# Optimization experiments

Hardware: AMD Instinct MI355X
Metric: run time of the kernel (lower is better)

The kernel has to match this reference:

```python
import jax, jax.numpy as jnp
import numpy as np

# Dimensions: d_model D, heads H, head dim DH (H*DH==D), resonator freqs NF, FFN rank R
B, T, D, H, DH, NF, R = 2, 1024, 1024, 16, 64, 256, 4096
EPS_LN = 1e-5
EPS_ATTN = 1e-6


def setup_inputs() -> dict:
    key = jax.random.key(0)
    ks = jax.random.split(key, 16)
    n = lambda i, shape, s=0.02: jax.random.normal(ks[i], shape, dtype=jnp.float32) * s
    return {
        "x": jax.random.normal(ks[0], (B, T, D), dtype=jnp.float32),
        # resonator input projections
        "W_amp": n(1, (D, NF)), "b_amp": jnp.zeros((NF,), jnp.float32),
        "W_phi": n(2, (D, NF)), "b_phi": jnp.zeros((NF,), jnp.float32),
        # resonator dynamics: per-frequency rotation, retention logit, firing threshold
        "omega": jax.random.uniform(ks[3], (NF,), dtype=jnp.float32, minval=0.0, maxval=float(np.pi)),
        "ret_logit": jnp.full((NF,), 2.0, jnp.float32),
        "theta": jnp.full((NF,), 0.5, jnp.float32),
        # feat_proj: 3*NF -> D
        "W_feat": n(4, (3 * NF, D)), "b_feat": jnp.zeros((D,), jnp.float32),
        # linear attention projections (BDH-GPU style, relu feature map, no out proj)
        "Wq": n(5, (D, H * DH)), "Wk": n(6, (D, H * DH)), "Wv": n(7, (D, H * DH)),
        # per-head layernorm affine
        "lnh_w": jnp.ones((H, DH), jnp.float32), "lnh_b": jnp.zeros((H, DH), jnp.float32),
        # ReLU low-rank FFN (positive_out=True)
        "W1": n(8, (D, R)), "b1": jnp.zeros((R,), jnp.float32),
        "W2": n(9, (R, D)), "b2": jnp.zeros((D,), jnp.float32),
        # final layernorm
        "ln_w": jnp.ones((D,), jnp.float32), "ln_b": jnp.zeros((D,), jnp.float32),
    }


def reference(x, W_amp, b_amp, W_phi, b_phi, omega, ret_logit, theta,
              W_feat, b_feat, Wq, Wk, Wv, lnh_w, lnh_b,
              W1, b1, W2, b2, ln_w, ln_b):
    Bb, Tt, Dd = x.shape
    # --- resonator input field: complex polar(amp, phi) ---
    amp = jax.nn.softplus(x @ W_amp + b_amp)                 # [B,T,NF]
    phi = jnp.float32(np.pi) * jnp.tanh(x @ W_phi + b_phi)   # [B,T,NF]
    u = jax.lax.complex(amp * jnp.cos(phi), amp * jnp.sin(phi))  # complex64 [B,T,NF]
    # --- sequential complex resonator recurrence (the kernel-headroom scan) ---
    decay = jax.nn.sigmoid(ret_logit)                         # [NF]
    a = jax.lax.complex(decay * jnp.cos(omega), decay * jnp.sin(omega))  # [NF] complex

    def step(X, u_t):
        pre = a * X + u_t                                     # [B,NF] complex
        g = jax.nn.sigmoid(jnp.abs(pre) - theta)              # threshold-map gate
        Xn = pre * g.astype(pre.dtype)
        return Xn, Xn

    X0 = jnp.zeros((Bb, u.shape[-1]), jnp.complex64)
    _, Xs = jax.lax.scan(step, X0, jnp.swapaxes(u, 0, 1))     # [T,B,NF]
    Xs = jnp.swapaxes(Xs, 0, 1)                               # [B,T,NF]
    feat = jnp.concatenate([Xs.real, Xs.imag, jnp.abs(Xs)], axis=-1)  # [B,T,3NF]
    h = jax.nn.relu(feat @ W_feat + b_feat)                   # pos(feat_proj(feat)) -> [B,T,D]
    # --- causal linear attention (relu feature map, cumulative KV state) ---
    q = jax.nn.relu(h @ Wq).reshape(Bb, Tt, H, DH)
    k = jax.nn.relu(h @ Wk).reshape(Bb, Tt, H, DH)
    v = (h @ Wv).reshape(Bb, Tt, H, DH)
    kv = jnp.cumsum(k[..., :, None] * v[..., None, :], axis=1)  # [B,T,H,DH,DH]
    ksum = jnp.cumsum(k, axis=1)                                 # [B,T,H,DH]
    num = jnp.einsum('bthd,bthde->bthe', q, kv)
    den = jnp.einsum('bthd,bthd->bth', q, ksum)[..., None] + EPS_ATTN
    y = num / den                                                # [B,T,H,DH]
    # --- per-head layernorm ---
    mean = y.mean(-1, keepdims=True)
    var = y.var(-1, keepdims=True)
    y = (y - mean) / jnp.sqrt(var + EPS_LN) * lnh_w + lnh_b
    y = y.reshape(Bb, Tt, H * DH)                                # [B,T,D]
    # --- ReLU low-rank FFN, positive_out ---
    y = jax.nn.relu(jax.nn.relu(y @ W1 + b1) @ W2 + b2)
    # --- residual + layernorm ---
    z = x + y
    mu = z.mean(-1, keepdims=True)
    vz = z.var(-1, keepdims=True)
    out = (z - mu) / jnp.sqrt(vz + EPS_LN) * ln_w + ln_b
    return out
```

## Files before the change

kernel.cpp:

```cpp
#include <hip/hip_runtime.h>
#include <hip/hip_bf16.h>
#include <math.h>

#ifndef M_PI_F
#define M_PI_F 3.14159265358979323846f
#endif

static constexpr int Bb = 2, Tt = 1024, Dd = 1024, Hh = 16, DHh = 64, NFf = 256, Rr = 4096;
static constexpr int Mm = Bb * Tt;
static constexpr int CHK = 64, NCHK = Tt / CHK;
static constexpr int QS = 3072;

enum Epi { EPI_NONE = 0, EPI_RELU, EPI_QKV };

typedef __attribute__((ext_vector_type(8))) short bf16x8;
typedef __attribute__((ext_vector_type(4))) float f32x4;

__device__ inline float bf2f(unsigned short u) {
  union { unsigned int i; float f; } c;
  c.i = (unsigned int)u << 16;
  return c.f;
}

__device__ inline void gload16(const short* g, short* l) {
  __builtin_amdgcn_global_load_lds(
      (const __attribute__((address_space(1))) unsigned int*)g,
      (__attribute__((address_space(3))) unsigned int*)l, 16, 0, 0);
}

#define GSTAGE(bufsel, kk0)                                           \
  _Pragma("unroll") for (int si = 0; si < 4; ++si) {                  \
    const int s = wid + si * 4;                                       \
    gload16(A + (size_t)(m0 + s * 8 + srow) * ldk + (kk0) + skk,      \
            &lA[(bufsel) * 8192 + s * 512]);                          \
    gload16(BT + (size_t)(n0 + s * 8 + srow) * ldk + (kk0) + skk,     \
            &lB[(bufsel) * 8192 + s * 512]);                          \
  }

template <int EPI, int OUTBF, int SPLITK>
__global__ __launch_bounds__(256) void gemm_mfma(const short* __restrict__ A,
                                                 const short* __restrict__ BT,
                                                 const float* __restrict__ bias,
                                                 float* __restrict__ Cf,
                                                 __hip_bfloat16* __restrict__ Cb,
                                                 int M, int N, int ldk) {
  __shared__ short lA[2 * 128 * 64];
  __shared__ short lB[2 * 128 * 64];
  const int tid = threadIdx.x;
  const int wid = tid >> 6, lane = tid & 63;

  const int nwg = gridDim.x * gridDim.y;
  const int wg = blockIdx.y * gridDim.x + blockIdx.x;
  const int qq = nwg >> 3, rr = nwg & 7;
  const int xcd = wg & 7, idx = wg >> 3;
  const int wg2 = (xcd < rr ? xcd * (qq + 1) : rr * (qq + 1) + (xcd - rr) * qq) + idx;
  const int bx = wg2 % gridDim.x, by = wg2 / gridDim.x;

  const int m0 = by * 128, n0 = bx * 128;
  const int wm = (wid >> 1) * 64, wn = (wid & 1) * 64;
  const int srow = lane >> 3;
  const int skk = (((lane & 7) ^ (lane >> 3)) << 3);

  int kstart = 0, klen = ldk;
  if (SPLITK > 1) {
    klen = ldk / SPLITK;
    kstart = blockIdx.z * klen;
    if (OUTBF)
      Cb += (size_t)blockIdx.z * M * N;
    else
      Cf += (size_t)blockIdx.z * M * N;
  }
  const int kend = kstart + klen;

  f32x4 acc[4][4] = {};

  GSTAGE(0, kstart);
  int cur = 0;
  for (int k0 = kstart; k0 < kend; k0 += 64) {
    if (k0 + 64 < kend) {
      GSTAGE(cur ^ 1, k0 + 64);
      asm volatile("s_waitcnt vmcnt(8)" ::: "memory");
    } else {
      asm volatile("s_waitcnt vmcnt(0)" ::: "memory");
    }
    asm volatile("s_barrier" ::: "memory");
    const short* bA = &lA[cur * 8192];
    const short* bB = &lB[cur * 8192];
#pragma unroll
    for (int kk = 0; kk < 2; ++kk) {
      const int krd = kk * 32 + (lane >> 4) * 8;
      const int rsel = lane & 15;
      const int kswz = krd ^ ((rsel & 7) << 3);
      bf16x8 af[4], bfr[4];
#pragma unroll
      for (int i = 0; i < 4; ++i) {
        af[i] = *(const bf16x8*)&bA[(wm + i * 16 + rsel) * 64 + kswz];
        bfr[i] = *(const bf16x8*)&bB[(wn + i * 16 + rsel) * 64 + kswz];
      }
#pragma unroll
      for (int i = 0; i < 4; ++i)
#pragma unroll
        for (int j = 0; j < 4; ++j)
          acc[i][j] = __builtin_amdgcn_mfma_f32_16x16x32_bf16(af[i], bfr[j], acc[i][j], 0, 0, 0);
    }
    asm volatile("s_barrier" ::: "memory");
    cur ^= 1;
  }

  const int crow = (lane >> 4) * 4;
  const int ccol = lane & 15;
#pragma unroll
  for (int j = 0; j < 4; ++j) {
    const int col = n0 + wn + j * 16 + ccol;
    const float bv = bias ? bias[col] : 0.f;
#pragma unroll
    for (int i = 0; i < 4; ++i) {
#pragma unroll
      for (int r = 0; r < 4; ++r) {
        float v = acc[i][j][r] + bv;
        const int row = m0 + wm + i * 16 + crow + r;
        if (EPI == EPI_QKV) {
          const float vv = (col < 2048) ? fmaxf(v, 0.f) : v;
          Cb[(size_t)row * QS + col] = __float2bfloat16(vv);
        } else {
          if (EPI == EPI_RELU) v = fmaxf(v, 0.f);
          const size_t off = (size_t)row * N + col;
          if (OUTBF)
            Cb[off] = __float2bfloat16(v);
          else
            Cf[off] = v;
        }
      }
    }
  }
}

__global__ __launch_bounds__(256) void reduce_polar(const __hip_bfloat16* __restrict__ part,
                                                    const float* __restrict__ b_amp,
                                                    const float* __restrict__ b_phi,
                                                    __hip_bfloat16* __restrict__ outr,
                                                    __hip_bfloat16* __restrict__ outi) {
  const int idx = blockIdx.x * 256 + threadIdx.x;
  const int row = idx >> 8, c = idx & 255;
  const size_t MN = (size_t)Mm * 512;
  const size_t pa = (size_t)row * 512 + c;
  const unsigned short* pu = (const unsigned short*)part;
  float a = bf2f(pu[pa]) + bf2f(pu[pa + MN]) + bf2f(pu[pa + 2 * MN]) + bf2f(pu[pa + 3 * MN]) +
            b_amp[c];
  float ph = bf2f(pu[pa + 256]) + bf2f(pu[pa + 256 + MN]) + bf2f(pu[pa + 256 + 2 * MN]) +
             bf2f(pu[pa + 256 + 3 * MN]) + b_phi[c];
  a = (a > 0.f) ? (a + log1pf(expf(-a))) : log1pf(expf(a));
  ph = M_PI_F * tanhf(ph);
  float s, co;
  sincosf(ph, &s, &co);
  outr[idx] = __float2bfloat16(a * co);
  outi[idx] = __float2bfloat16(a * s);
}

struct TCDesc {
  const float* src[8];
  __hip_bfloat16* dst[8];
  const float* x;
  __hip_bfloat16* xb;
};

__global__ __launch_bounds__(256) void transpose_cast_all(TCDesc d) {
  constexpr int KS[8] = {1024, 1024, 768, 1024, 1024, 1024, 1024, 4096};
  constexpr int NS[8] = {256, 256, 1024, 1024, 1024, 1024, 4096, 1024};
  constexpr int CUM[9] = {0, 256, 512, 1280, 2304, 3328, 4352, 8448, 12544};
  const int bid = blockIdx.x;
  if (bid >= 12544) {
    const int i = ((bid - 12544) * 256 + threadIdx.x) * 4;
    const float4 v = *(const float4*)&d.x[i];
    d.xb[i + 0] = __float2bfloat16(v.x);
    d.xb[i + 1] = __float2bfloat16(v.y);
    d.xb[i + 2] = __float2bfloat16(v.z);
    d.xb[i + 3] = __float2bfloat16(v.w);
    return;
  }
  __shared__ float tile[32][33];
  int w = 0;
#pragma unroll
  for (int i = 0; i < 8; ++i)
    if (bid >= CUM[i + 1]) w = i + 1;
  const int tlocal = bid - CUM[w];
  const int K = KS[w], N = NS[w];
  const int tilesN = N / 32;
  const int bk = (tlocal / tilesN) * 32, bn = (tlocal % tilesN) * 32;
  const float* W = d.src[w];
  __hip_bfloat16* WT = d.dst[w];
  const int tx = threadIdx.x & 31, ty = threadIdx.x >> 5;
#pragma unroll
  for (int r = 0; r < 32; r += 8) tile[ty + r][tx] = W[(size_t)(bk + ty + r) * N + bn + tx];
  __syncthreads();
#pragma unroll
  for (int r = 0; r < 32; r += 8)
    WT[(size_t)(bn + ty + r) * K + bk + tx] = __float2bfloat16(tile[tx][ty + r]);
}

static constexpr int RES_P = 16;
static constexpr int RES_TC = 128;
static constexpr int RES_W = 128;

#define RES_LOAD(buf_r, buf_i, tg)                                        \
  if ((tg) < cend) {                                                      \
    _Pragma("unroll") for (int i = 0; i < RES_P; ++i) {                   \
      buf_r[i] = __bfloat162float(ur[bbase + (size_t)((tg) + i) * NFf]);  \
      buf_i[i] = __bfloat162float(ui[bbase + (size_t)((tg) + i) * NFf]);  \
    }                                                                     \
  }

#define RES_STEP(buf_r, buf_i, tg)                                      \
  {                                                                      \
    const bool wr_ = (tg) >= cstart;                                     \
    _Pragma("unroll") for (int i = 0; i < RES_P; ++i) {                  \
      const float pr = fmaf(ar, Xr, fmaf(-ai, Xi, buf_r[i]));            \
      const float pim = fmaf(ar, Xi, fmaf(ai, Xr, buf_i[i]));            \
      const float mag = __builtin_amdgcn_sqrtf(fmaf(pr, pr, pim * pim)); \
      const float g = __builtin_amdgcn_rcpf(1.f + __expf(th - mag));     \
      Xr = pr * g;                                                       \
      Xi = pim * g;                                                      \
      if (wr_) {                                                         \
        const size_t fb = ((size_t)b * Tt + (tg) + i) * (3 * NFf);       \
        featb[fb + f] = __float2bfloat16(Xr);                            \
        featb[fb + NFf + f] = __float2bfloat16(Xi);                      \
        featb[fb + 2 * NFf + f] = __float2bfloat16(mag * g);             \
      }                                                                  \
    }                                                                    \
  }

__global__ __launch_bounds__(64) void resonator_scan(const __hip_bfloat16* __restrict__ ur,
                                                     const __hip_bfloat16* __restrict__ ui,
                                                     const float* __restrict__ omega,
                                                     const float* __restrict__ ret_logit,
                                                     const float* __restrict__ theta,
                                                     __hip_bfloat16* __restrict__ featb) {
  const int bid = blockIdx.x;
  const int tc = bid & 7;
  const int fs = (bid >> 3) & 3;
  const int b = bid >> 5;
  const int f = fs * 64 + threadIdx.x;
  const int cstart = tc * RES_TC;
  const int cend = cstart + RES_TC;
  const int tbeg = (cstart >= RES_W) ? cstart - RES_W : 0;

  const float dec = 1.f / (1.f + __expf(-ret_logit[f]));
  float so, co;
  sincosf(omega[f], &so, &co);
  const float ar = dec * co, ai = dec * so;
  const float th = theta[f];
  const size_t bbase = (size_t)b * Tt * NFf + f;
  float Xr = 0.f, Xi = 0.f;
  float Ar[RES_P], Ai[RES_P], Br[RES_P], Bi[RES_P];
  RES_LOAD(Ar, Ai, tbeg);
  for (int t0 = tbeg; t0 < cend; t0 += 2 * RES_P) {
    RES_LOAD(Br, Bi, t0 + RES_P);
    RES_STEP(Ar, Ai, t0);
    RES_LOAD(Ar, Ai, t0 + 2 * RES_P);
    RES_STEP(Br, Bi, t0 + RES_P);
  }
}

__global__ __launch_bounds__(256) void attn_chunk_kv(const __hip_bfloat16* __restrict__ k,
                                                     const __hip_bfloat16* __restrict__ v,
                                                     float* __restrict__ S,
                                                     float* __restrict__ Ksum) {
  __shared__ float Ks[64][68], Vs[64][68];
  const int g = blockIdx.x;
  const int j = g & (NCHK - 1), bh = g >> 4;
  const int b = bh >> 4, h = bh & (Hh - 1);
  const int tid = threadIdx.x;
  const size_t rowbase = (size_t)(b * Tt + j * CHK) * QS + h * DHh;
  const unsigned short* ku = (const unsigned short*)k;
  const unsigned short* vu = (const unsigned short*)v;
  for (int l = tid; l < 4096; l += 256) {
    const int s = l >> 6, d = l & 63;
    Ks[s][d] = bf2f(ku[rowbase + (size_t)s * QS + d]);
    Vs[s][d] = bf2f(vu[rowbase + (size_t)s * QS + d]);
  }
  __syncthreads();
  const int d0 = tid & 63, eb = tid >> 6, e0 = eb * 16;
  float4 acc4[4] = {};
  float ks = 0.f;
  for (int s = 0; s < 64; ++s) {
    const float kd = Ks[s][d0];
    ks += kd;
#pragma unroll
    for (int i = 0; i < 4; ++i) {
      const float4 v4 = *(const float4*)&Vs[s][e0 + 4 * i];
      acc4[i].x = fmaf(kd, v4.x, acc4[i].x);
      acc4[i].y = fmaf(kd, v4.y, acc4[i].y);
      acc4[i].z = fmaf(kd, v4.z, acc4[i].z);
      acc4[i].w = fmaf(kd, v4.w, acc4[i].w);
    }
  }
  float* Sg = S + (size_t)g * 4096 + (size_t)d0 * 64 + e0;
#pragma unroll
  for (int i = 0; i < 4; ++i) *(float4*)&Sg[4 * i] = acc4[i];
  if (eb == 0) Ksum[(size_t)g * 64 + d0] = ks;
}

__global__ __launch_bounds__(256) void attn_prefix(float* __restrict__ S,
                                                   float* __restrict__ Ksum) {
  const int bid = blockIdx.x;
  const int tid = threadIdx.x;
  if (bid < 512) {
    const int bh = bid >> 4, r = bid & 15;
    const int de = r * 256 + tid;
    const size_t base = (size_t)bh * (NCHK * 4096) + de;
    float vv[NCHK];
#pragma unroll
    for (int j = 0; j < NCHK; ++j) vv[j] = S[base + (size_t)j * 4096];
    float run = 0.f;
#pragma unroll
    for (int j = 0; j < NCHK; ++j) {
      const float tmp = vv[j];
      S[base + (size_t)j * 4096] = run;
      run += tmp;
    }
  } else {
    const int cid = (bid - 512) * 256 + tid;
    const int bh = cid >> 6, d = cid & 63;
    const size_t base = (size_t)bh * (NCHK * 64) + d;
    float vv[NCHK];
#pragma unroll
    for (int j = 0; j < NCHK; ++j) vv[j] = Ksum[base + (size_t)j * 64];
    float run = 0.f;
#pragma unroll
    for (int j = 0; j < NCHK; ++j) {
      const float tmp = vv[j];
      Ksum[base + (size_t)j * 64] = run;
      run += tmp;
    }
  }
}

__global__ __launch_bounds__(256) void attn_out(const __hip_bfloat16* __restrict__ q,
                                                const __hip_bfloat16* __restrict__ k,
                                                const __hip_bfloat16* __restrict__ v,
                                                const float* __restrict__ S,
                                                const float* __restrict__ Ksum,
                                                const float* __restrict__ lnw,
                                                const float* __restrict__ lnb,
                                                __hip_bfloat16* __restrict__ yhb) {
  __shared__ float Qt[64][65];
  __shared__ float KVP[64][68];
  __shared__ float At[64][65];
  const int g = blockIdx.x;
  const int j = g & (NCHK - 1), bh = g >> 4;
  const int b = bh >> 4, h = bh & (Hh - 1);
  const int tid = threadIdx.x;
  const size_t rowbase = (size_t)(b * Tt + j * CHK) * QS + h * DHh;
  const unsigned short* qu = (const unsigned short*)q;
  const unsigned short* ku = (const unsigned short*)k;
  const unsigned short* vu = (const unsigned short*)v;
  for (int l = tid; l < 4096; l += 256) {
    const int s = l >> 6, d = l & 63;
    Qt[d][s] = bf2f(qu[rowbase + (size_t)s * QS + d]);
    KVP[s][d] = bf2f(ku[rowbase + (size_t)s * QS + d]);
  }
  __syncthreads();
  const int t = tid >> 2, sg = tid & 3;
  const float* pk = Ksum + (size_t)g * 64;
  float adot[16] = {};
  float qpk = 0.f;
  for (int c = 0; c < 16; ++c) {
    const float q0 = Qt[4 * c + 0][t], q1 = Qt[4 * c + 1][t];
    const float q2 = Qt[4 * c + 2][t], q3 = Qt[4 * c + 3][t];
    const float4 pk4 = *(const float4*)&pk[4 * c];
    qpk = fmaf(q0, pk4.x, fmaf(q1, pk4.y, fmaf(q2, pk4.z, fmaf(q3, pk4.w, qpk))));
#pragma unroll
    for (int i = 0; i < 16; ++i) {
      const float4 k4 = *(const float4*)&KVP[sg * 16 + i][4 * c];
      adot[i] = fmaf(q0, k4.x, fmaf(q1, k4.y, fmaf(q2, k4.z, fmaf(q3, k4.w, adot[i]))));
    }
  }
  float rs = 0.f;
#pragma unroll
  for (int i = 0; i < 16; ++i) {
    if (sg * 16 + i > t) adot[i] = 0.f;
    rs += adot[i];
  }
  rs += __shfl_xor(rs, 1);
  rs += __shfl_xor(rs, 2);
  const float den = qpk + rs + 1e-6f;
  __syncthreads();
#pragma unroll
  for (int i = 0; i < 16; ++i) At[sg * 16 + i][t] = adot[i];
  for (int l = tid; l < 4096; l += 256) {
    const int s = l >> 6, d = l & 63;
    KVP[s][d] = bf2f(vu[rowbase + (size_t)s * QS + d]);
  }
  __syncthreads();
  const int e0 = sg * 16;
  float4 num[4] = {};
  for (int s = 0; s <= t; ++s) {
    const float av = At[s][t];
#pragma unroll
    for (int i = 0; i < 4; ++i) {
      const float4 v4 = *(const float4*)&KVP[s][e0 + 4 * i];
      num[i].x = fmaf(av, v4.x, num[i].x);
      num[i].y = fmaf(av, v4.y, num[i].y);
      num[i].z = fmaf(av, v4.z, num[i].z);
      num[i].w = fmaf(av, v4.w, num[i].w);
    }
  }
  __syncthreads();
  const float* Pg = S + (size_t)g * 4096;
  for (int l = tid; l < 4096; l += 256) KVP[l >> 6][l & 63] = Pg[l];
  __syncthreads();
  for (int d = 0; d < 64; ++d) {
    const float qd = Qt[d][t];
#pragma unroll
    for (int i = 0; i < 4; ++i) {
      const float4 p4 = *(const float4*)&KVP[d][e0 + 4 * i];
      num[i].x = fmaf(qd, p4.x, num[i].x);
      num[i].y = fmaf(qd, p4.y, num[i].y);
      num[i].z = fmaf(qd, p4.z, num[i].z);
      num[i].w = fmaf(qd, p4.w, num[i].w);
    }
  }
  const float inv = 1.f / den;
  float o[16];
#pragma unroll
  for (int i = 0; i < 4; ++i) {
    o[4 * i + 0] = num[i].x * inv;
    o[4 * i + 1] = num[i].y * inv;
    o[4 * i + 2] = num[i].z * inv;
    o[4 * i + 3] = num[i].w * inv;
  }
  float s1 = 0.f, s2 = 0.f;
#pragma unroll
  for (int i = 0; i < 16; ++i) {
    s1 += o[i];
    s2 += o[i] * o[i];
  }
  s1 += __shfl_xor(s1, 1);
  s1 += __shfl_xor(s1, 2);
  s2 += __shfl_xor(s2, 1);
  s2 += __shfl_xor(s2, 2);
  const float mean = s1 * (1.f / 64.f);
  const float var = s2 * (1.f / 64.f) - mean * mean;
  const float rsv = rsqrtf(var + 1e-5f);
  const float* wv = lnw + h * DHh + e0;
  const float* bv = lnb + h * DHh + e0;
  unsigned short ob[16];
#pragma unroll
  for (int i = 0; i < 16; ++i) {
    const float r = (o[i] - mean) * rsv * wv[i] + bv[i];
    __hip_bfloat16 hv = __float2bfloat16(r);
    ob[i] = *(unsigned short*)&hv;
  }
  unsigned short* yg =
      (unsigned short*)yhb + (size_t)(b * Tt + j * CHK + t) * Dd + h * DHh + e0;
#pragma unroll
  for (int i = 0; i < 4; ++i) *(ushort4*)&yg[4 * i] = *(ushort4*)&ob[4 * i];
}

__global__ __launch_bounds__(256) void final_ln(const float* __restrict__ x,
                                                const __hip_bfloat16* __restrict__ part,
                                                const float* __restrict__ b2,
                                                const float* __restrict__ w,
                                                const float* __restrict__ bb,
                                                float* __restrict__ out) {
  __shared__ float r1[4], r2[4];
  const int row = blockIdx.x;
  const int tid = threadIdx.x;
  const size_t off = (size_t)row * Dd + tid * 4;
  const size_t MN = (size_t)Mm * Dd;
  float acc4[4] = {0.f, 0.f, 0.f, 0.f};
#pragma unroll
  for (int z = 0; z < 4; ++z) {
    const ushort4 u = *(const ushort4*)&part[off + (size_t)z * MN];
    acc4[0] += bf2f(u.x);
    acc4[1] += bf2f(u.y);
    acc4[2] += bf2f(u.z);
    acc4[3] += bf2f(u.w);
  }
  const float4 bv = *(const float4*)&b2[tid * 4];
  const float4 xa = *(const float4*)&x[off];
  float z[4];
  z[0] = xa.x + fmaxf(acc4[0] + bv.x, 0.f);
  z[1] = xa.y + fmaxf(acc4[1] + bv.y, 0.f);
  z[2] = xa.z + fmaxf(acc4[2] + bv.z, 0.f);
  z[3] = xa.w + fmaxf(acc4[3] + bv.w, 0.f);
  float s1 = z[0] + z[1] + z[2] + z[3];
  float s2 = z[0] * z[0] + z[1] * z[1] + z[2] * z[2] + z[3] * z[3];
#pragma unroll
  for (int o = 1; o < 64; o <<= 1) {
    s1 += __shfl_xor(s1, o);
    s2 += __shfl_xor(s2, o);
  }
  const int wid = tid >> 6;
  if ((tid & 63) == 0) {
    r1[wid] = s1;
    r2[wid] = s2;
  }
  __syncthreads();
  const float t1 = r1[0] + r1[1] + r1[2] + r1[3];
  const float t2 = r2[0] + r2[1] + r2[2] + r2[3];
  const float mu = t1 * (1.f / Dd);
  const float var = t2 * (1.f / Dd) - mu * mu;
  const float rsv = rsqrtf(var + 1e-5f);
  float4 o4;
  float* op = &o4.x;
#pragma unroll
  for (int jj = 0; jj < 4; ++jj) op[jj] = (z[jj] - mu) * rsv * w[tid * 4 + jj] + bb[tid * 4 + jj];
  *(float4*)&out[off] = o4;
}

extern "C" void kernel_launch(void* const* d_in, const int* in_sizes, int n_in,
                              void* d_out, int out_size, void* d_ws, size_t ws_size,
                              hipStream_t stream) {
  const float* x = (const float*)d_in[0];
  const float* W_amp = (const float*)d_in[1];
  const float* b_amp = (const float*)d_in[2];
  const float* W_phi = (const float*)d_in[3];
  const float* b_phi = (const float*)d_in[4];
  const float* omega = (const float*)d_in[5];
  const float* ret_logit = (const float*)d_in[6];
  const float* theta = (const float*)d_in[7];
  const float* W_feat = (const float*)d_in[8];
  const float* b_feat = (const float*)d_in[9];
  const float* Wq = (const float*)d_in[10];
  const float* Wk = (const float*)d_in[11];
  const float* Wv = (const float*)d_in[12];
  const float* lnh_w = (const float*)d_in[13];
  const float* lnh_b = (const float*)d_in[14];
  const float* W1 = (const float*)d_in[15];
  const float* b1 = (const float*)d_in[16];
  const float* W2 = (const float*)d_in[17];
  const float* b2 = (const float*)d_in[18];
  const float* ln_w = (const float*)d_in[19];
  const float* ln_b = (const float*)d_in[20];

  char* p = (char*)d_ws;
  auto alloc = [&](size_t bytes) {
    char* r = p;
    p += (bytes + 255) & ~(size_t)255;
    return r;
  };
  __hip_bfloat16* xb = (__hip_bfloat16*)alloc((size_t)Mm * Dd * 2);
  __hip_bfloat16* urh = (__hip_bfloat16*)alloc((size_t)Mm * NFf * 2);
  __hip_bfloat16* uih = (__hip_bfloat16*)alloc((size_t)Mm * NFf * 2);
  __hip_bfloat16* WTamp = (__hip_bfloat16*)alloc((size_t)NFf * Dd * 2);
  __hip_bfloat16* WTphi = (__hip_bfloat16*)alloc((size_t)NFf * Dd * 2);
  __hip_bfloat16* WTfeat = (__hip_bfloat16*)alloc((size_t)Dd * 3 * NFf * 2);
  __hip_bfloat16* WTq = (__hip_bfloat16*)alloc((size_t)Dd * Dd * 2);
  __hip_bfloat16* WTk = (__hip_bfloat16*)alloc((size_t)Dd * Dd * 2);
  __hip_bfloat16* WTv = (__hip_bfloat16*)alloc((size_t)Dd * Dd * 2);
  __hip_bfloat16* WT1 = (__hip_bfloat16*)alloc((size_t)Rr * Dd * 2);
  __hip_bfloat16* WT2 = (__hip_bfloat16*)alloc((size_t)Dd * Rr * 2);
  __hip_bfloat16* hb = (__hip_bfloat16*)alloc((size_t)Mm * Dd * 2);
  __hip_bfloat16* qkvb = (__hip_bfloat16*)alloc((size_t)Mm * QS * 2);
  __hip_bfloat16* yhb = (__hip_bfloat16*)alloc((size_t)Mm * Dd * 2);
  float* S = (float*)alloc((size_t)Bb * Hh * NCHK * 4096 * 4);
  float* Ksum = (float*)alloc((size_t)Bb * Hh * NCHK * 64 * 4);
  __hip_bfloat16* f1b = (__hip_bfloat16*)alloc((size_t)Mm * Rr * 2);

  __hip_bfloat16* featb = xb;
  const __hip_bfloat16* q = qkvb;
  const __hip_bfloat16* k = qkvb + 1024;
  const __hip_bfloat16* v = qkvb + 2048;
  __hip_bfloat16* pamp = qkvb;
  __hip_bfloat16* partial = qkvb;
  float* out = (float*)d_out;

  const dim3 blk(256);

  TCDesc tc;
  tc.src[0] = W_amp; tc.dst[0] = WTamp;
  tc.src[1] = W_phi; tc.dst[1] = WTphi;
  tc.src[2] = W_feat; tc.dst[2] = WTfeat;
  tc.src[3] = Wq; tc.dst[3] = WTq;
  tc.src[4] = Wk; tc.dst[4] = WTk;
  tc.src[5] = Wv; tc.dst[5] = WTv;
  tc.src[6] = W1; tc.dst[6] = WT1;
  tc.src[7] = W2; tc.dst[7] = WT2;
  tc.x = x; tc.xb = xb;
  transpose_cast_all<<<dim3(12544 + 2048), blk, 0, stream>>>(tc);

  gemm_mfma<EPI_NONE, 1, 4><<<dim3(512 / 128, Mm / 128, 4), blk, 0, stream>>>(
      (const short*)xb, (const short*)WTamp, nullptr, nullptr, pamp, Mm, 512, Dd);
  reduce_polar<<<dim3(Mm * NFf / 256), blk, 0, stream>>>(pamp, b_amp, b_phi, urh, uih);

  resonator_scan<<<dim3(64), dim3(64), 0, stream>>>(urh, uih, omega, ret_logit, theta, featb);

  gemm_mfma<EPI_RELU, 1, 0><<<dim3(Dd / 128, Mm / 128), blk, 0, stream>>>(
      (const short*)featb, (const short*)WTfeat, b_feat, nullptr, hb, Mm, Dd, 3 * NFf);

  gemm_mfma<EPI_QKV, 1, 0><<<dim3(QS / 128, Mm / 128), blk, 0, stream>>>(
      (const short*)hb, (const short*)WTq, nullptr, nullptr, qkvb, Mm, QS, Dd);

  attn_chunk_kv<<<dim3(Bb * Hh * NCHK), blk, 0, stream>>>(k, v, S, Ksum);
  attn_prefix<<<dim3(520), blk, 0, stream>>>(S, Ksum);
  attn_out<<<dim3(Bb * Hh * NCHK), blk, 0, stream>>>(q, k, v, S, Ksum, lnh_w, lnh_b, yhb);

  gemm_mfma<EPI_RELU, 1, 0><<<dim3(Rr / 128, Mm / 128), blk, 0, stream>>>(
      (const short*)yhb, (const short*)WT1, b1, nullptr, f1b, Mm, Rr, Dd);

  gemm_mfma<EPI_NONE, 1, 4><<<dim3(Dd / 128, Mm / 128, 4), blk, 0, stream>>>(
      (const short*)f1b, (const short*)WT2, nullptr, nullptr, partial, Mm, Dd, Rr);

  final_ln<<<dim3(Mm), blk, 0, stream>>>(x, partial, b2, ln_w, ln_b, out);
}
```

Before: 195.5 us.

## Overlap resonator scan with weight transpose-casts in one combined launch

Splits the weight transpose/cast kernel so only W_amp, W_phi and x are converted before the first GEMM. The remaining weight transposes run in the same launch as the latency-bound resonator scan, which uses only 64 blocks, so the idle CUs do the casting work while the scan runs. Split-K partial buffers get their own allocations instead of aliasing qkvb, because qkvb is no longer free at those points. The scan blocks now launch with 256 threads and 192 return immediately. Scan blocks could also be scheduled behind many transpose blocks, which may delay the critical path.

After: 187.0 us. -4.3%, faster.

```diff
diff --git a/kernel.cpp b/kernel.cpp
--- a/kernel.cpp
+++ b/kernel.cpp
@@ -133,6 +133,43 @@
       }
     }
   }
+}
+
+__device__ __forceinline__ void tc_tile(float (*tile)[33], const float* __restrict__ W,
+                                        __hip_bfloat16* __restrict__ WT, int K, int N,
+                                        int tlocal) {
+  const int tilesN = N / 32;
+  const int bk = (tlocal / tilesN) * 32, bn = (tlocal % tilesN) * 32;
+  const int tx = threadIdx.x & 31, ty = threadIdx.x >> 5;
+#pragma unroll
+  for (int r = 0; r < 32; r += 8) tile[ty + r][tx] = W[(size_t)(bk + ty + r) * N + bn + tx];
+  __syncthreads();
+#pragma unroll
+  for (int r = 0; r < 32; r += 8)
+    WT[(size_t)(bn + ty + r) * K + bk + tx] = __float2bfloat16(tile[tx][ty + r]);
+}
+
+__global__ __launch_bounds__(256) void tc_first(const float* __restrict__ W_amp,
+                                                const float* __restrict__ W_phi,
+                                                __hip_bfloat16* __restrict__ WTamp,
+                                                __hip_bfloat16* __restrict__ WTphi,
+                                                const float* __restrict__ x,
+                                                __hip_bfloat16* __restrict__ xb) {
+  __shared__ float tile[32][33];
+  const int bid = blockIdx.x;
+  if (bid >= 512) {
+    const int i = ((bid - 512) * 256 + threadIdx.x) * 4;
+    const float4 v = *(const float4*)&x[i];
+    xb[i + 0] = __float2bfloat16(v.x);
+    xb[i + 1] = __float2bfloat16(v.y);
+    xb[i + 2] = __float2bfloat16(v.z);
+    xb[i + 3] = __float2bfloat16(v.w);
+    return;
+  }
+  if (bid < 256)
+    tc_tile(tile, W_amp, WTamp, 1024, 256, bid);
+  else
+    tc_tile(tile, W_phi, WTphi, 1024, 256, bid - 256);
 }
 
 __global__ __launch_bounds__(256) void reduce_polar(const __hip_bfloat16* __restrict__ part,
@@ -157,47 +194,6 @@
   outi[idx] = __float2bfloat16(a * s);
 }
 
-struct TCDesc {
-  const float* src[8];
-  __hip_bfloat16* dst[8];
-  const float* x;
-  __hip_bfloat16* xb;
-};
-
-__global__ __launch_bounds__(256) void transpose_cast_all(TCDesc d) {
-  constexpr int KS[8] = {1024, 1024, 768, 1024, 1024, 1024, 1024, 4096};
-  constexpr int NS[8] = {256, 256, 1024, 1024, 1024, 1024, 4096, 1024};
-  constexpr int CUM[9] = {0, 256, 512, 1280, 2304, 3328, 4352, 8448, 12544};
-  const int bid = blockIdx.x;
-  if (bid >= 12544) {
-    const int i = ((bid - 12544) * 256 + threadIdx.x) * 4;
-    const float4 v = *(const float4*)&d.x[i];
-    d.xb[i + 0] = __float2bfloat16(v.x);
-    d.xb[i + 1] = __float2bfloat16(v.y);
-    d.xb[i + 2] = __float2bfloat16(v.z);
-    d.xb[i + 3] = __float2bfloat16(v.w);
-    return;
-  }
-  __shared__ float tile[32][33];
-  int w = 0;
-#pragma unroll
-  for (int i = 0; i < 8; ++i)
-    if (bid >= CUM[i + 1]) w = i + 1;
-  const int tlocal = bid - CUM[w];
-  const int K = KS[w], N = NS[w];
-  const int tilesN = N / 32;
-  const int bk = (tlocal / tilesN) * 32, bn = (tlocal % tilesN) * 32;
-  const float* W = d.src[w];
-  __hip_bfloat16* WT = d.dst[w];
-  const int tx = threadIdx.x & 31, ty = threadIdx.x >> 5;
-#pragma unroll
-  for (int r = 0; r < 32; r += 8) tile[ty + r][tx] = W[(size_t)(bk + ty + r) * N + bn + tx];
-  __syncthreads();
-#pragma unroll
-  for (int r = 0; r < 32; r += 8)
-    WT[(size_t)(bn + ty + r) * K + bk + tx] = __float2bfloat16(tile[tx][ty + r]);
-}
-
 static constexpr int RES_P = 16;
 static constexpr int RES_TC = 128;
 static constexpr int RES_W = 128;
@@ -229,36 +225,58 @@
     }                                                                    \
   }
 
-__global__ __launch_bounds__(64) void resonator_scan(const __hip_bfloat16* __restrict__ ur,
-                                                     const __hip_bfloat16* __restrict__ ui,
-                                                     const float* __restrict__ omega,
-                                                     const float* __restrict__ ret_logit,
-                                                     const float* __restrict__ theta,
-                                                     __hip_bfloat16* __restrict__ featb) {
+struct STDesc {
+  const float* src[6];
+  __hip_bfloat16* dst[6];
+  const __hip_bfloat16* ur;
+  const __hip_bfloat16* ui;
+  const float* omega;
+  const float* ret_logit;
+  const float* theta;
+  __hip_bfloat16* featb;
+};
+
+__global__ __launch_bounds__(256) void scan_and_tc(STDesc d) {
+  __shared__ float tile[32][33];
   const int bid = blockIdx.x;
-  const int tc = bid & 7;
-  const int fs = (bid >> 3) & 3;
-  const int b = bid >> 5;
-  const int f = fs * 64 + threadIdx.x;
-  const int cstart = tc * RES_TC;
-  const int cend = cstart + RES_TC;
-  const int tbeg = (cstart >= RES_W) ? cstart - RES_W : 0;
-
-  const float dec = 1.f / (1.f + __expf(-ret_logit[f]));
-  float so, co;
-  sincosf(omega[f], &so, &co);
-  const float ar = dec * co, ai = dec * so;
-  const float th = theta[f];
-  const size_t bbase = (size_t)b * Tt * NFf + f;
-  float Xr = 0.f, Xi = 0.f;
-  float Ar[RES_P], Ai[RES_P], Br[RES_P], Bi[RES_P];
-  RES_LOAD(Ar, Ai, tbeg);
-  for (int t0 = tbeg; t0 < cend; t0 += 2 * RES_P) {
-    RES_LOAD(Br, Bi, t0 + RES_P);
-    RES_STEP(Ar, Ai, t0);
-    RES_LOAD(Ar, Ai, t0 + 2 * RES_P);
-    RES_STEP(Br, Bi, t0 + RES_P);
-  }
+  if (bid < 64) {
+    if (threadIdx.x >= 64) return;
+    const int tc = bid & 7;
+    const int fs = (bid >> 3) & 3;
+    const int b = bid >> 5;
+    const int f = fs * 64 + threadIdx.x;
+    const int cstart = tc * RES_TC;
+    const int cend = cstart + RES_TC;
+    const int tbeg = (cstart >= RES_W) ? cstart - RES_W : 0;
+    const __hip_bfloat16* ur = d.ur;
+    const __hip_bfloat16* ui = d.ui;
+    __hip_bfloat16* featb = d.featb;
+    const float dec = 1.f / (1.f + __expf(-d.ret_logit[f]));
+    float so, co;
+    sincosf(d.omega[f], &so, &co);
+    const float ar = dec * co, ai = dec * so;
+    const float th = d.theta[f];
+    const size_t bbase = (size_t)b * Tt * NFf + f;
+    float Xr = 0.f, Xi = 0.f;
+    float Ar[RES_P], Ai[RES_P], Br[RES_P], Bi[RES_P];
+    RES_LOAD(Ar, Ai, tbeg);
+    for (int t0 = tbeg; t0 < cend; t0 += 2 * RES_P) {
+      RES_LOAD(Br, Bi, t0 + RES_P);
+      RES_STEP(Ar, Ai, t0);
+      RES_LOAD(Ar, Ai, t0 + 2 * RES_P);
+      RES_STEP(Br, Bi, t0 + RES_P);
+    }
+    return;
+  }
+  constexpr int KS[6] = {768, 1024, 1024, 1024, 1024, 4096};
+  constexpr int NS[6] = {1024, 1024, 1024, 1024, 4096, 1024};
+  constexpr int CUM[7] = {0, 768, 1792, 2816, 3840, 7936, 12032};
+  const int t = bid - 64;
+  int w = 0;
+#pragma unroll
+  for (int i = 0; i < 6; ++i)
+    if (t >= CUM[i + 1]) w = i + 1;
+  tc_tile(tile, d.src[w], d.dst[w], KS[w], NS[w], t - CUM[w]);
 }
 
 __global__ __launch_bounds__(256) void attn_chunk_kv(const __hip_bfloat16* __restrict__ k,
@@ -557,34 +575,34 @@
   float* S = (float*)alloc((size_t)Bb * Hh * NCHK * 4096 * 4);
   float* Ksum = (float*)alloc((size_t)Bb * Hh * NCHK * 64 * 4);
   __hip_bfloat16* f1b = (__hip_bfloat16*)alloc((size_t)Mm * Rr * 2);
+  __hip_bfloat16* pamp = (__hip_bfloat16*)alloc((size_t)4 * Mm * 512 * 2);
+  __hip_bfloat16* pffn2 = (__hip_bfloat16*)alloc((size_t)4 * Mm * Dd * 2);
 
   __hip_bfloat16* featb = xb;
   const __hip_bfloat16* q = qkvb;
   const __hip_bfloat16* k = qkvb + 1024;
   const __hip_bfloat16* v = qkvb + 2048;
-  __hip_bfloat16* pamp = qkvb;
-  __hip_bfloat16* partial = qkvb;
   float* out = (float*)d_out;
 
   const dim3 blk(256);
 
-  TCDesc tc;
-  tc.src[0] = W_amp; tc.dst[0] = WTamp;
-  tc.src[1] = W_phi; tc.dst[1] = WTphi;
-  tc.src[2] = W_feat; tc.dst[2] = WTfeat;
-  tc.src[3] = Wq; tc.dst[3] = WTq;
-  tc.src[4] = Wk; tc.dst[4] = WTk;
-  tc.src[5] = Wv; tc.dst[5] = WTv;
-  tc.src[6] = W1; tc.dst[6] = WT1;
-  tc.src[7] = W2; tc.dst[7] = WT2;
-  tc.x = x; tc.xb = xb;
-  transpose_cast_all<<<dim3(12544 + 2048), blk, 0, stream>>>(tc);
+  tc_first<<<dim3(2560), blk, 0, stream>>>(W_amp, W_phi, WTamp, WTphi, x, xb);
 
   gemm_mfma<EPI_NONE, 1, 4><<<dim3(512 / 128, Mm / 128, 4), blk, 0, stream>>>(
       (const short*)xb, (const short*)WTamp, nullptr, nullptr, pamp, Mm, 512, Dd);
   reduce_polar<<<dim3(Mm * NFf / 256), blk, 0, stream>>>(pamp, b_amp, b_phi, urh, uih);
 
-  resonator_scan<<<dim3(64), dim3(64), 0, stream>>>(urh, uih, omega, ret_logit, theta, featb);
+  STDesc st;
+  st.src[0] = W_feat; st.dst[0] = WTfeat;
+  st.src[1] = Wq; st.dst[1] = WTq;
+  st.src[2] = Wk; st.dst[2] = WTk;
+  st.src[3] = Wv; st.dst[3] = WTv;
+  st.src[4] = W1; st.dst[4] = WT1;
+  st.src[5] = W2; st.dst[5] = WT2;
+  st.ur = urh; st.ui = uih;
+  st.omega = omega; st.ret_logit = ret_logit; st.theta = theta;
+  st.featb = featb;
+  scan_and_tc<<<dim3(64 + 12032), blk, 0, stream>>>(st);
 
   gemm_mfma<EPI_RELU, 1, 0><<<dim3(Dd / 128, Mm / 128), blk, 0, stream>>>(
       (const short*)featb, (const short*)WTfeat, b_feat, nullptr, hb, Mm, Dd, 3 * NFf);
@@ -600,7 +618,7 @@
       (const short*)yhb, (const short*)WT1, b1, nullptr, f1b, Mm, Rr, Dd);
 
   gemm_mfma<EPI_NONE, 1, 4><<<dim3(Dd / 128, Mm / 128, 4), blk, 0, stream>>>(
-      (const short*)f1b, (const short*)WT2, nullptr, nullptr, partial, Mm, Dd, Rr);
-
-  final_ln<<<dim3(Mm), blk, 0, stream>>>(x, partial, b2, ln_w, ln_b, out);
-}
+      (const short*)f1b, (const short*)WT2, nullptr, nullptr, pffn2, Mm, Dd, Rr);
+
+  final_ln<<<dim3(Mm), blk, 0, stream>>>(x, pffn2, b2, ln_w, ln_b, out);
+}
```
